# Kernel tuning notes

Measured on AMD Instinct MI355X. Metric: run time of the kernel, lower is better.

The kernel has to match this reference:

```python
import jax, jax.numpy as jnp
import numpy as np

B, T = 32, 2048            # batch, longest acoustic length
SIN, HIN = 1024, 1024      # decoder-state dim, listener-output dim
KD, VD = 512, 512          # key/value projection dims
EPS = 1e-12                # F.normalize eps


def setup_inputs() -> dict:
    key = jax.random.key(0)
    ks = jax.random.split(key, 9)
    s = 0.02
    return {
        "decoder_state": jax.random.normal(ks[0], (B, SIN), dtype=jnp.float32),
        "listener_output": jax.random.normal(ks[1], (B, T, HIN), dtype=jnp.float32),
        "outputs_length": jax.random.randint(ks[2], (B,), 1, T + 1, dtype=jnp.int32),
        "Ws": jax.random.normal(ks[3], (KD, SIN), dtype=jnp.float32) * s,
        "bs": jnp.zeros((KD,), dtype=jnp.float32),
        "Wh": jax.random.normal(ks[4], (KD, HIN), dtype=jnp.float32) * s,
        "bh": jnp.zeros((KD,), dtype=jnp.float32),
        "Wv": jax.random.normal(ks[5], (VD, HIN), dtype=jnp.float32) * s,
        "bv": jnp.zeros((VD,), dtype=jnp.float32),
    }


def reference(decoder_state, listener_output, outputs_length, Ws, bs, Wh, bh, Wv, bv):
    # query: [B, KD]
    query = decoder_state @ Ws.T + bs
    # key: [B, T, KD]
    keyp = jnp.einsum('bth,kh->btk', listener_output, Wh) + bh
    # energy: [B, 1, T]
    energy = jnp.einsum('bk,btk->bt', query, keyp)[:, None, :]
    attn = jax.nn.softmax(energy, axis=2)
    # length mask; NOTE: original loop skips i==0, so sample 0 is never masked
    pos = jnp.arange(T)
    mask = (pos[None, :] < outputs_length[:, None]).astype(attn.dtype)
    mask = mask.at[0].set(1.0)
    attn = attn * mask[:, None, :]
    # L1 renormalize (F.normalize p=1, dim=2, eps=1e-12); attn >= 0
    attn = attn / jnp.maximum(jnp.sum(attn, axis=2, keepdims=True), EPS)
    # value: [B, T, VD]; context: [B, VD]
    value = jnp.einsum('bth,vh->btv', listener_output, Wv) + bv
    context = jnp.einsum('bqt,btv->bqv', attn, value)[:, 0, :]
    return context, attn
```

## Files before the change

### kernel.cpp

```cpp
#include <hip/hip_runtime.h>
#include <math.h>

#define BB 32
#define TT 2048
#define SIN 1024
#define HIN 1024
#define KD 512
#define VD 512

#define OFF_Q      0
#define OFF_WPART  16384
#define OFF_W      147456
#define OFF_E      180224
#define OFF_PART   245760
#define OFF_CTX    772096
#define OFF_R      804864

__device__ __forceinline__ float dot4(float4 a, float4 b) {
  return fmaf(a.x, b.x, fmaf(a.y, b.y, fmaf(a.z, b.z, a.w * b.w)));
}

__device__ __forceinline__ float wave_reduce_sum(float e) {
#pragma unroll
  for (int off = 32; off > 0; off >>= 1) e += __shfl_xor(e, off, 64);
  return e;
}

__global__ __launch_bounds__(256) void k_query(const float* __restrict__ ds,
                                               const float* __restrict__ Ws,
                                               const float* __restrict__ bs,
                                               float* __restrict__ q) {
  const int lane = threadIdx.x & 63;
  const int wid  = threadIdx.x >> 6;
  const int k    = blockIdx.x * 4 + wid;
  const float4* Wr = (const float4*)(Ws + (size_t)k * SIN);
  float4 w0 = Wr[lane], w1 = Wr[64 + lane], w2 = Wr[128 + lane], w3 = Wr[192 + lane];
  float bk = bs[k];
  for (int b = 0; b < BB; ++b) {
    const float4* dr = (const float4*)(ds + (size_t)b * SIN);
    float4 d0 = dr[lane], d1 = dr[64 + lane], d2 = dr[128 + lane], d3 = dr[192 + lane];
    float e = dot4(w0, d0) + dot4(w1, d1) + dot4(w2, d2) + dot4(w3, d3);
    e = wave_reduce_sum(e);
    if (lane == 0) q[(size_t)b * KD + k] = e + bk;
  }
}

__global__ __launch_bounds__(256) void k_wpart(const float* __restrict__ Wh,
                                               const float* __restrict__ q,
                                               float* __restrict__ wpart) {
  __shared__ float qs[8][128];
  const int h  = blockIdx.x * 256 + threadIdx.x;
  const int b0 = blockIdx.y * 8;
  const int k0 = blockIdx.z * 128;
#pragma unroll
  for (int r = 0; r < 4; ++r) {
    int lin = r * 256 + threadIdx.x;
    qs[lin >> 7][lin & 127] = q[(size_t)(b0 + (lin >> 7)) * KD + k0 + (lin & 127)];
  }
  __syncthreads();
  float acc[8] = {0.f, 0.f, 0.f, 0.f, 0.f, 0.f, 0.f, 0.f};
  for (int kk = 0; kk < 128; ++kk) {
    float wh = Wh[(size_t)(k0 + kk) * HIN + h];
#pragma unroll
    for (int i = 0; i < 8; ++i) acc[i] = fmaf(wh, qs[i][kk], acc[i]);
  }
#pragma unroll
  for (int i = 0; i < 8; ++i)
    wpart[(size_t)blockIdx.z * (BB * HIN) + (size_t)(b0 + i) * HIN + h] = acc[i];
}

__global__ __launch_bounds__(256) void k_wred(const float* __restrict__ wpart,
                                              float* __restrict__ w) {
  const int b = blockIdx.x;
#pragma unroll
  for (int i = 0; i < 4; ++i) {
    int h = threadIdx.x + 256 * i;
    float s = 0.f;
#pragma unroll
    for (int z = 0; z < 4; ++z) s += wpart[(size_t)z * (BB * HIN) + (size_t)b * HIN + h];
    w[(size_t)b * HIN + h] = s;
  }
}

__global__ __launch_bounds__(256) void k_main(const float* __restrict__ L,
                                              const float* __restrict__ wv,
                                              const int* __restrict__ lens,
                                              float* __restrict__ energy,
                                              float* __restrict__ part) {
  const int b     = blockIdx.x >> 4;
  const int chunk = blockIdx.x & 15;
  const int wid   = threadIdx.x >> 6;
  const int lane  = threadIdx.x & 63;
  const int len   = lens[b];
  const bool row0 = (b == 0);

  const float4* wr = (const float4*)(wv + (size_t)b * HIN);
  float4 w0 = wr[lane], w1 = wr[64 + lane], w2 = wr[128 + lane], w3 = wr[192 + lane];

  float m = -INFINITY, z = 0.f, kept = 0.f;
  float4 a0 = {0, 0, 0, 0}, a1 = {0, 0, 0, 0}, a2 = {0, 0, 0, 0}, a3 = {0, 0, 0, 0};
  const size_t rowbase = (size_t)b * TT * HIN;

  for (int i = 0; i < 32; ++i) {
    const int t = chunk * 128 + i * 4 + wid;
    const float4* vr = (const float4*)(L + rowbase + (size_t)t * HIN);
    float4 v0 = vr[lane], v1 = vr[64 + lane], v2 = vr[128 + lane], v3 = vr[192 + lane];
    float e = dot4(w0, v0) + dot4(w1, v1) + dot4(w2, v2) + dot4(w3, v3);
    e = wave_reduce_sum(e);
    if (lane == 0) energy[(size_t)b * TT + t] = e;
    if (e > m) {
      float sc = __expf(m - e);
      z *= sc; kept *= sc;
      a0.x *= sc; a0.y *= sc; a0.z *= sc; a0.w *= sc;
      a1.x *= sc; a1.y *= sc; a1.z *= sc; a1.w *= sc;
      a2.x *= sc; a2.y *= sc; a2.z *= sc; a2.w *= sc;
      a3.x *= sc; a3.y *= sc; a3.z *= sc; a3.w *= sc;
      m = e;
    }
    float p = __expf(e - m);
    z += p;
    if (row0 || t < len) {
      kept += p;
      a0.x = fmaf(p, v0.x, a0.x); a0.y = fmaf(p, v0.y, a0.y);
      a0.z = fmaf(p, v0.z, a0.z); a0.w = fmaf(p, v0.w, a0.w);
      a1.x = fmaf(p, v1.x, a1.x); a1.y = fmaf(p, v1.y, a1.y);
      a1.z = fmaf(p, v1.z, a1.z); a1.w = fmaf(p, v1.w, a1.w);
      a2.x = fmaf(p, v2.x, a2.x); a2.y = fmaf(p, v2.y, a2.y);
      a2.z = fmaf(p, v2.z, a2.z); a2.w = fmaf(p, v2.w, a2.w);
      a3.x = fmaf(p, v3.x, a3.x); a3.y = fmaf(p, v3.y, a3.y);
      a3.z = fmaf(p, v3.z, a3.z); a3.w = fmaf(p, v3.w, a3.w);
    }
  }

  __shared__ float hdr[4][3];
  __shared__ float accs[4][1024];
  if (lane == 0) { hdr[wid][0] = m; hdr[wid][1] = z; hdr[wid][2] = kept; }
  float4* as = (float4*)accs[wid];
  as[lane] = a0; as[64 + lane] = a1; as[128 + lane] = a2; as[192 + lane] = a3;
  __syncthreads();
  float M = fmaxf(fmaxf(hdr[0][0], hdr[1][0]), fmaxf(hdr[2][0], hdr[3][0]));
  float sc_[4]; float Z = 0.f, K = 0.f;
#pragma unroll
  for (int w = 0; w < 4; ++w) {
    float s = __expf(hdr[w][0] - M);
    sc_[w] = s; Z = fmaf(hdr[w][1], s, Z); K = fmaf(hdr[w][2], s, K);
  }
  float* pb = part + (size_t)blockIdx.x * 1028;
  if (threadIdx.x == 0) { pb[0] = M; pb[1] = Z; pb[2] = K; }
#pragma unroll
  for (int i = 0; i < 4; ++i) {
    int h = threadIdx.x + 256 * i;
    float A = accs[0][h] * sc_[0] + accs[1][h] * sc_[1] +
              accs[2][h] * sc_[2] + accs[3][h] * sc_[3];
    pb[4 + h] = A;
  }
}

__global__ __launch_bounds__(256) void k_reduce(const float* __restrict__ part,
                                                const float* __restrict__ energy,
                                                const int* __restrict__ lens,
                                                float* __restrict__ ctx,
                                                float* __restrict__ rb,
                                                float* __restrict__ out_attn) {
  const int b = blockIdx.x;
  __shared__ float sM[16], sZ[16], sK[16];
  if (threadIdx.x < 16) {
    const float* pb = part + (size_t)(b * 16 + threadIdx.x) * 1028;
    sM[threadIdx.x] = pb[0]; sZ[threadIdx.x] = pb[1]; sK[threadIdx.x] = pb[2];
  }
  __syncthreads();
  float M = -INFINITY;
#pragma unroll
  for (int i = 0; i < 16; ++i) M = fmaxf(M, sM[i]);
  float scl[16]; float Z = 0.f, K = 0.f;
#pragma unroll
  for (int i = 0; i < 16; ++i) {
    float s = __expf(sM[i] - M);
    scl[i] = s; Z = fmaf(sZ[i], s, Z); K = fmaf(sK[i], s, K);
  }
  const float kept_sum = K / Z;
  const float ks = fmaxf(kept_sum, 1e-12f);
  const float inv = 1.f / (Z * ks);
#pragma unroll
  for (int i = 0; i < 4; ++i) {
    int h = threadIdx.x + 256 * i;
    float A = 0.f;
#pragma unroll
    for (int p = 0; p < 16; ++p)
      A = fmaf(part[(size_t)(b * 16 + p) * 1028 + 4 + h], scl[p], A);
    ctx[(size_t)b * HIN + h] = A * inv;
  }
  const int len = lens[b];
#pragma unroll
  for (int i = 0; i < 8; ++i) {
    int t = threadIdx.x + 256 * i;
    bool keep = (b == 0) || (t < len);
    float e = energy[(size_t)b * TT + t];
    out_attn[(size_t)b * TT + t] = keep ? __expf(e - M) * inv : 0.f;
  }
  if (threadIdx.x == 0) rb[b] = kept_sum / ks;
}

__global__ __launch_bounds__(256) void k_context(const float* __restrict__ Wvm,
                                                 const float* __restrict__ bv,
                                                 const float* __restrict__ ctx,
                                                 const float* __restrict__ rb,
                                                 float* __restrict__ out) {
  const int lane = threadIdx.x & 63;
  const int wid  = threadIdx.x >> 6;
  const int v    = blockIdx.x * 4 + wid;
  const float4* Wr = (const float4*)(Wvm + (size_t)v * HIN);
  float4 w0 = Wr[lane], w1 = Wr[64 + lane], w2 = Wr[128 + lane], w3 = Wr[192 + lane];
  const float bvv = bv[v];
  for (int b = 0; b < BB; ++b) {
    const float4* cr = (const float4*)(ctx + (size_t)b * HIN);
    float4 c0 = cr[lane], c1 = cr[64 + lane], c2 = cr[128 + lane], c3 = cr[192 + lane];
    float e = dot4(w0, c0) + dot4(w1, c1) + dot4(w2, c2) + dot4(w3, c3);
    e = wave_reduce_sum(e);
    if (lane == 0) out[(size_t)b * VD + v] = e + bvv * rb[b];
  }
}

extern "C" void kernel_launch(void* const* d_in, const int* in_sizes, int n_in,
                              void* d_out, int out_size, void* d_ws, size_t ws_size,
                              hipStream_t stream) {
  const float* ds   = (const float*)d_in[0];
  const float* L    = (const float*)d_in[1];
  const int*   lens = (const int*)d_in[2];
  const float* Ws   = (const float*)d_in[3];
  const float* bs   = (const float*)d_in[4];
  const float* Wh   = (const float*)d_in[5];
  const float* Wv   = (const float*)d_in[7];
  const float* bv   = (const float*)d_in[8];
  float* out = (float*)d_out;
  float* ws  = (float*)d_ws;

  float* q      = ws + OFF_Q;
  float* wpart  = ws + OFF_WPART;
  float* w      = ws + OFF_W;
  float* energy = ws + OFF_E;
  float* part   = ws + OFF_PART;
  float* ctx    = ws + OFF_CTX;
  float* rbuf   = ws + OFF_R;

  k_query  <<<128, 256, 0, stream>>>(ds, Ws, bs, q);
  k_wpart  <<<dim3(4, 4, 4), 256, 0, stream>>>(Wh, q, wpart);
  k_wred   <<<32, 256, 0, stream>>>(wpart, w);
  k_main   <<<512, 256, 0, stream>>>(L, w, lens, energy, part);
  k_reduce <<<32, 256, 0, stream>>>(part, energy, lens, ctx, rbuf, out + BB * VD);
  k_context<<<128, 256, 0, stream>>>(Wv, bv, ctx, rbuf, out);
}
```

Before: 450.3 us.

## Split fused online-softmax pass into energy, softmax, and weighted-sum kernels

After: 480.5 us. 1.07x slower.

```diff
diff --git a/kernel.cpp b/kernel.cpp
--- a/kernel.cpp
+++ b/kernel.cpp
@@ -13,17 +13,11 @@
 #define OFF_W      147456
 #define OFF_E      180224
 #define OFF_PART   245760
-#define OFF_CTX    772096
-#define OFF_R      804864
+#define OFF_CTX    1294336
+#define OFF_R      1327104
 
 __device__ __forceinline__ float dot4(float4 a, float4 b) {
   return fmaf(a.x, b.x, fmaf(a.y, b.y, fmaf(a.z, b.z, a.w * b.w)));
-}
-
-__device__ __forceinline__ float wave_reduce_sum(float e) {
-#pragma unroll
-  for (int off = 32; off > 0; off >>= 1) e += __shfl_xor(e, off, 64);
-  return e;
 }
 
 __global__ __launch_bounds__(256) void k_query(const float* __restrict__ ds,
@@ -38,9 +32,10 @@
   float bk = bs[k];
   for (int b = 0; b < BB; ++b) {
     const float4* dr = (const float4*)(ds + (size_t)b * SIN);
-    float4 d0 = dr[lane], d1 = dr[64 + lane], d2 = dr[128 + lane], d3 = dr[192 + lane];
-    float e = dot4(w0, d0) + dot4(w1, d1) + dot4(w2, d2) + dot4(w3, d3);
-    e = wave_reduce_sum(e);
+    float e = dot4(w0, dr[lane]) + dot4(w1, dr[64 + lane]) +
+              dot4(w2, dr[128 + lane]) + dot4(w3, dr[192 + lane]);
+#pragma unroll
+    for (int off = 32; off > 0; off >>= 1) e += __shfl_xor(e, off, 64);
     if (lane == 0) q[(size_t)b * KD + k] = e + bk;
   }
 }
@@ -82,123 +77,149 @@
   }
 }
 
-__global__ __launch_bounds__(256) void k_main(const float* __restrict__ L,
-                                              const float* __restrict__ wv,
-                                              const int* __restrict__ lens,
-                                              float* __restrict__ energy,
-                                              float* __restrict__ part) {
-  const int b     = blockIdx.x >> 4;
-  const int chunk = blockIdx.x & 15;
+__global__ __launch_bounds__(256) void k_energy(const float* __restrict__ L,
+                                                const float* __restrict__ wv,
+                                                float* __restrict__ energy) {
+  const int b     = blockIdx.x >> 5;
+  const int chunk = blockIdx.x & 31;
   const int wid   = threadIdx.x >> 6;
   const int lane  = threadIdx.x & 63;
-  const int len   = lens[b];
-  const bool row0 = (b == 0);
-
   const float4* wr = (const float4*)(wv + (size_t)b * HIN);
   float4 w0 = wr[lane], w1 = wr[64 + lane], w2 = wr[128 + lane], w3 = wr[192 + lane];
-
-  float m = -INFINITY, z = 0.f, kept = 0.f;
-  float4 a0 = {0, 0, 0, 0}, a1 = {0, 0, 0, 0}, a2 = {0, 0, 0, 0}, a3 = {0, 0, 0, 0};
-  const size_t rowbase = (size_t)b * TT * HIN;
-
-  for (int i = 0; i < 32; ++i) {
-    const int t = chunk * 128 + i * 4 + wid;
-    const float4* vr = (const float4*)(L + rowbase + (size_t)t * HIN);
-    float4 v0 = vr[lane], v1 = vr[64 + lane], v2 = vr[128 + lane], v3 = vr[192 + lane];
-    float e = dot4(w0, v0) + dot4(w1, v1) + dot4(w2, v2) + dot4(w3, v3);
-    e = wave_reduce_sum(e);
-    if (lane == 0) energy[(size_t)b * TT + t] = e;
-    if (e > m) {
-      float sc = __expf(m - e);
-      z *= sc; kept *= sc;
-      a0.x *= sc; a0.y *= sc; a0.z *= sc; a0.w *= sc;
-      a1.x *= sc; a1.y *= sc; a1.z *= sc; a1.w *= sc;
-      a2.x *= sc; a2.y *= sc; a2.z *= sc; a2.w *= sc;
-      a3.x *= sc; a3.y *= sc; a3.z *= sc; a3.w *= sc;
-      m = e;
+  const size_t rowbase4 = ((size_t)b * TT + chunk * 64) * 256;
+  const int t0 = wid * 16;
+#pragma unroll
+  for (int g = 0; g < 4; ++g) {
+    const int t = t0 + g * 4;
+    const float4* r0 = (const float4*)L + rowbase4 + (size_t)t * 256;
+    const float4* r1 = r0 + 256;
+    const float4* r2 = r0 + 512;
+    const float4* r3 = r0 + 768;
+    float e0 = dot4(w0, r0[lane]) + dot4(w1, r0[64 + lane]) +
+               dot4(w2, r0[128 + lane]) + dot4(w3, r0[192 + lane]);
+    float e1 = dot4(w0, r1[lane]) + dot4(w1, r1[64 + lane]) +
+               dot4(w2, r1[128 + lane]) + dot4(w3, r1[192 + lane]);
+    float e2 = dot4(w0, r2[lane]) + dot4(w1, r2[64 + lane]) +
+               dot4(w2, r2[128 + lane]) + dot4(w3, r2[192 + lane]);
+    float e3 = dot4(w0, r3[lane]) + dot4(w1, r3[64 + lane]) +
+               dot4(w2, r3[128 + lane]) + dot4(w3, r3[192 + lane]);
+#pragma unroll
+    for (int off = 32; off > 0; off >>= 1) {
+      e0 += __shfl_xor(e0, off, 64);
+      e1 += __shfl_xor(e1, off, 64);
+      e2 += __shfl_xor(e2, off, 64);
+      e3 += __shfl_xor(e3, off, 64);
     }
-    float p = __expf(e - m);
-    z += p;
-    if (row0 || t < len) {
-      kept += p;
-      a0.x = fmaf(p, v0.x, a0.x); a0.y = fmaf(p, v0.y, a0.y);
-      a0.z = fmaf(p, v0.z, a0.z); a0.w = fmaf(p, v0.w, a0.w);
-      a1.x = fmaf(p, v1.x, a1.x); a1.y = fmaf(p, v1.y, a1.y);
-      a1.z = fmaf(p, v1.z, a1.z); a1.w = fmaf(p, v1.w, a1.w);
-      a2.x = fmaf(p, v2.x, a2.x); a2.y = fmaf(p, v2.y, a2.y);
-      a2.z = fmaf(p, v2.z, a2.z); a2.w = fmaf(p, v2.w, a2.w);
-      a3.x = fmaf(p, v3.x, a3.x); a3.y = fmaf(p, v3.y, a3.y);
-      a3.z = fmaf(p, v3.z, a3.z); a3.w = fmaf(p, v3.w, a3.w);
+    if (lane == 0) {
+      float4 ev = {e0, e1, e2, e3};
+      *(float4*)(energy + (size_t)b * TT + chunk * 64 + t) = ev;
     }
   }
-
-  __shared__ float hdr[4][3];
-  __shared__ float accs[4][1024];
-  if (lane == 0) { hdr[wid][0] = m; hdr[wid][1] = z; hdr[wid][2] = kept; }
-  float4* as = (float4*)accs[wid];
-  as[lane] = a0; as[64 + lane] = a1; as[128 + lane] = a2; as[192 + lane] = a3;
-  __syncthreads();
-  float M = fmaxf(fmaxf(hdr[0][0], hdr[1][0]), fmaxf(hdr[2][0], hdr[3][0]));
-  float sc_[4]; float Z = 0.f, K = 0.f;
-#pragma unroll
-  for (int w = 0; w < 4; ++w) {
-    float s = __expf(hdr[w][0] - M);
-    sc_[w] = s; Z = fmaf(hdr[w][1], s, Z); K = fmaf(hdr[w][2], s, K);
-  }
-  float* pb = part + (size_t)blockIdx.x * 1028;
-  if (threadIdx.x == 0) { pb[0] = M; pb[1] = Z; pb[2] = K; }
-#pragma unroll
-  for (int i = 0; i < 4; ++i) {
-    int h = threadIdx.x + 256 * i;
-    float A = accs[0][h] * sc_[0] + accs[1][h] * sc_[1] +
-              accs[2][h] * sc_[2] + accs[3][h] * sc_[3];
-    pb[4 + h] = A;
-  }
-}
-
-__global__ __launch_bounds__(256) void k_reduce(const float* __restrict__ part,
-                                                const float* __restrict__ energy,
-                                                const int* __restrict__ lens,
-                                                float* __restrict__ ctx,
-                                                float* __restrict__ rb,
-                                                float* __restrict__ out_attn) {
-  const int b = blockIdx.x;
-  __shared__ float sM[16], sZ[16], sK[16];
-  if (threadIdx.x < 16) {
-    const float* pb = part + (size_t)(b * 16 + threadIdx.x) * 1028;
-    sM[threadIdx.x] = pb[0]; sZ[threadIdx.x] = pb[1]; sK[threadIdx.x] = pb[2];
-  }
-  __syncthreads();
-  float M = -INFINITY;
-#pragma unroll
-  for (int i = 0; i < 16; ++i) M = fmaxf(M, sM[i]);
-  float scl[16]; float Z = 0.f, K = 0.f;
-#pragma unroll
-  for (int i = 0; i < 16; ++i) {
-    float s = __expf(sM[i] - M);
-    scl[i] = s; Z = fmaf(sZ[i], s, Z); K = fmaf(sK[i], s, K);
-  }
+}
+
+__global__ __launch_bounds__(256) void k_softmax(const float* __restrict__ energy,
+                                                 const int* __restrict__ lens,
+                                                 float* __restrict__ attn,
+                                                 float* __restrict__ rb) {
+  const int b   = blockIdx.x;
+  const int tid = threadIdx.x;
+  const int wid = tid >> 6;
+  const int len = lens[b];
+  const bool row0 = (b == 0);
+  const float4* e4 = (const float4*)(energy + (size_t)b * TT);
+  float4 ea = e4[tid], eb = e4[256 + tid];
+
+  __shared__ float red[4];
+  float m = fmaxf(fmaxf(fmaxf(ea.x, ea.y), fmaxf(ea.z, ea.w)),
+                  fmaxf(fmaxf(eb.x, eb.y), fmaxf(eb.z, eb.w)));
+#pragma unroll
+  for (int off = 32; off > 0; off >>= 1) m = fmaxf(m, __shfl_xor(m, off, 64));
+  if ((tid & 63) == 0) red[wid] = m;
+  __syncthreads();
+  const float M = fmaxf(fmaxf(red[0], red[1]), fmaxf(red[2], red[3]));
+  __syncthreads();
+
+  float pa[4], pb[4];
+  pa[0] = __expf(ea.x - M); pa[1] = __expf(ea.y - M);
+  pa[2] = __expf(ea.z - M); pa[3] = __expf(ea.w - M);
+  pb[0] = __expf(eb.x - M); pb[1] = __expf(eb.y - M);
+  pb[2] = __expf(eb.z - M); pb[3] = __expf(eb.w - M);
+  const int ta = tid * 4, tb = 1024 + tid * 4;
+  float z = 0.f, kk = 0.f;
+#pragma unroll
+  for (int j = 0; j < 4; ++j) {
+    z += pa[j] + pb[j];
+    if (row0 || ta + j < len) kk += pa[j];
+    if (row0 || tb + j < len) kk += pb[j];
+  }
+#pragma unroll
+  for (int off = 32; off > 0; off >>= 1) {
+    z  += __shfl_xor(z, off, 64);
+    kk += __shfl_xor(kk, off, 64);
+  }
+  __shared__ float redZ[4], redK[4];
+  if ((tid & 63) == 0) { redZ[wid] = z; redK[wid] = kk; }
+  __syncthreads();
+  const float Z = redZ[0] + redZ[1] + redZ[2] + redZ[3];
+  const float K = redK[0] + redK[1] + redK[2] + redK[3];
   const float kept_sum = K / Z;
   const float ks = fmaxf(kept_sum, 1e-12f);
   const float inv = 1.f / (Z * ks);
-#pragma unroll
-  for (int i = 0; i < 4; ++i) {
-    int h = threadIdx.x + 256 * i;
-    float A = 0.f;
-#pragma unroll
-    for (int p = 0; p < 16; ++p)
-      A = fmaf(part[(size_t)(b * 16 + p) * 1028 + 4 + h], scl[p], A);
-    ctx[(size_t)b * HIN + h] = A * inv;
-  }
-  const int len = lens[b];
-#pragma unroll
-  for (int i = 0; i < 8; ++i) {
-    int t = threadIdx.x + 256 * i;
-    bool keep = (b == 0) || (t < len);
-    float e = energy[(size_t)b * TT + t];
-    out_attn[(size_t)b * TT + t] = keep ? __expf(e - M) * inv : 0.f;
-  }
-  if (threadIdx.x == 0) rb[b] = kept_sum / ks;
+
+  float4 oa, ob;
+  oa.x = (row0 || ta + 0 < len) ? pa[0] * inv : 0.f;
+  oa.y = (row0 || ta + 1 < len) ? pa[1] * inv : 0.f;
+  oa.z = (row0 || ta + 2 < len) ? pa[2] * inv : 0.f;
+  oa.w = (row0 || ta + 3 < len) ? pa[3] * inv : 0.f;
+  ob.x = (row0 || tb + 0 < len) ? pb[0] * inv : 0.f;
+  ob.y = (row0 || tb + 1 < len) ? pb[1] * inv : 0.f;
+  ob.z = (row0 || tb + 2 < len) ? pb[2] * inv : 0.f;
+  ob.w = (row0 || tb + 3 < len) ? pb[3] * inv : 0.f;
+  float4* o4 = (float4*)(attn + (size_t)b * TT);
+  o4[tid] = oa; o4[256 + tid] = ob;
+  if (tid == 0) rb[b] = kept_sum / ks;
+}
+
+__global__ __launch_bounds__(256) void k_wsum(const float* __restrict__ L,
+                                              const float* __restrict__ attn,
+                                              float* __restrict__ part) {
+  const int b     = blockIdx.x >> 5;
+  const int chunk = blockIdx.x & 31;
+  const int tid   = threadIdx.x;
+  const size_t rowbase4 = ((size_t)b * TT + chunk * 64) * 256;
+  const float4* L4 = (const float4*)L + rowbase4;
+  const float* p = attn + (size_t)b * TT + chunk * 64;
+  float4 acc = {0.f, 0.f, 0.f, 0.f};
+#pragma unroll 4
+  for (int r = 0; r < 64; r += 4) {
+    float4 p4 = *(const float4*)(p + r);
+    float4 v0 = L4[(size_t)(r + 0) * 256 + tid];
+    float4 v1 = L4[(size_t)(r + 1) * 256 + tid];
+    float4 v2 = L4[(size_t)(r + 2) * 256 + tid];
+    float4 v3 = L4[(size_t)(r + 3) * 256 + tid];
+    acc.x = fmaf(p4.x, v0.x, acc.x); acc.y = fmaf(p4.x, v0.y, acc.y);
+    acc.z = fmaf(p4.x, v0.z, acc.z); acc.w = fmaf(p4.x, v0.w, acc.w);
+    acc.x = fmaf(p4.y, v1.x, acc.x); acc.y = fmaf(p4.y, v1.y, acc.y);
+    acc.z = fmaf(p4.y, v1.z, acc.z); acc.w = fmaf(p4.y, v1.w, acc.w);
+    acc.x = fmaf(p4.z, v2.x, acc.x); acc.y = fmaf(p4.z, v2.y, acc.y);
+    acc.z = fmaf(p4.z, v2.z, acc.z); acc.w = fmaf(p4.z, v2.w, acc.w);
+    acc.x = fmaf(p4.w, v3.x, acc.x); acc.y = fmaf(p4.w, v3.y, acc.y);
+    acc.z = fmaf(p4.w, v3.z, acc.z); acc.w = fmaf(p4.w, v3.w, acc.w);
+  }
+  ((float4*)part)[(size_t)blockIdx.x * 256 + tid] = acc;
+}
+
+__global__ __launch_bounds__(256) void k_wsum_red(const float* __restrict__ part,
+                                                  float* __restrict__ ctx) {
+  const int b   = blockIdx.x;
+  const int tid = threadIdx.x;
+  float4 s = {0.f, 0.f, 0.f, 0.f};
+#pragma unroll
+  for (int c = 0; c < 32; ++c) {
+    float4 v = ((const float4*)part)[(size_t)(b * 32 + c) * 256 + tid];
+    s.x += v.x; s.y += v.y; s.z += v.z; s.w += v.w;
+  }
+  ((float4*)ctx)[(size_t)b * 256 + tid] = s;
 }
 
 __global__ __launch_bounds__(256) void k_context(const float* __restrict__ Wvm,
@@ -214,9 +235,10 @@
   const float bvv = bv[v];
   for (int b = 0; b < BB; ++b) {
     const float4* cr = (const float4*)(ctx + (size_t)b * HIN);
-    float4 c0 = cr[lane], c1 = cr[64 + lane], c2 = cr[128 + lane], c3 = cr[192 + lane];
-    float e = dot4(w0, c0) + dot4(w1, c1) + dot4(w2, c2) + dot4(w3, c3);
-    e = wave_reduce_sum(e);
+    float e = dot4(w0, cr[lane]) + dot4(w1, cr[64 + lane]) +
+              dot4(w2, cr[128 + lane]) + dot4(w3, cr[192 + lane]);
+#pragma unroll
+    for (int off = 32; off > 0; off >>= 1) e += __shfl_xor(e, off, 64);
     if (lane == 0) out[(size_t)b * VD + v] = e + bvv * rb[b];
   }
 }
@@ -242,11 +264,14 @@
   float* part   = ws + OFF_PART;
   float* ctx    = ws + OFF_CTX;
   float* rbuf   = ws + OFF_R;
-
-  k_query  <<<128, 256, 0, stream>>>(ds, Ws, bs, q);
-  k_wpart  <<<dim3(4, 4, 4), 256, 0, stream>>>(Wh, q, wpart);
-  k_wred   <<<32, 256, 0, stream>>>(wpart, w);
-  k_main   <<<512, 256, 0, stream>>>(L, w, lens, energy, part);
-  k_reduce <<<32, 256, 0, stream>>>(part, energy, lens, ctx, rbuf, out + BB * VD);
-  k_context<<<128, 256, 0, stream>>>(Wv, bv, ctx, rbuf, out);
-}
+  float* attn   = out + BB * VD;
+
+  k_query   <<<128, 256, 0, stream>>>(ds, Ws, bs, q);
+  k_wpart   <<<dim3(4, 4, 4), 256, 0, stream>>>(Wh, q, wpart);
+  k_wred    <<<32, 256, 0, stream>>>(wpart, w);
+  k_energy  <<<1024, 256, 0, stream>>>(L, w, energy);
+  k_softmax <<<32, 256, 0, stream>>>(energy, lens, attn, rbuf);
+  k_wsum    <<<1024, 256, 0, stream>>>(L, attn, part);
+  k_wsum_red<<<32, 256, 0, stream>>>(part, ctx);
+  k_context <<<128, 256, 0, stream>>>(Wv, bv, ctx, rbuf, out);
+}
```
